# Optimization experiments

Measured on AMD Instinct MI355X. Metric: run time of the kernel, lower is better.

Reference implementation:

```python
import jax, jax.numpy as jnp
import numpy as np
from jax import lax

B, IN_C, OUT_C, Z_DIM, H, W = 16, 128, 128, 128, 64, 64
K, NUM_GROUPS, EPS = 3, 8, 1e-5


def setup_inputs() -> dict:
    key = jax.random.key(0)
    ks = jax.random.split(key, 10)
    s = 1.0 / np.sqrt(Z_DIM)
    return {
        "x": jax.random.normal(ks[0], (B, IN_C, H, W), dtype=jnp.float32),
        "z": jax.random.normal(ks[1], (B, Z_DIM), dtype=jnp.float32),
        # hypernet head for conv1: z_dim -> out_c*in_c*k*k
        "h1_w": jax.random.normal(ks[2], (Z_DIM, OUT_C * IN_C * K * K), dtype=jnp.float32) * s,
        "h1_b": jax.random.normal(ks[3], (OUT_C * IN_C * K * K,), dtype=jnp.float32) * 0.01,
        # hypernet head for conv2: z_dim -> out_c*out_c*k*k
        "h2_w": jax.random.normal(ks[4], (Z_DIM, OUT_C * OUT_C * K * K), dtype=jnp.float32) * s,
        "h2_b": jax.random.normal(ks[5], (OUT_C * OUT_C * K * K,), dtype=jnp.float32) * 0.01,
        "gamma1": jnp.ones((OUT_C,), dtype=jnp.float32),
        "beta1": jnp.zeros((OUT_C,), dtype=jnp.float32),
        "gamma2": jnp.ones((OUT_C,), dtype=jnp.float32),
        "beta2": jnp.zeros((OUT_C,), dtype=jnp.float32),
    }


def _per_sample_conv(x, w, stride, pad):
    # x: [B,C,H,W], w: [B,O,I,k,k] -> [B,O,H',W'] (per-sample weights)
    def one(xi, wi):
        return lax.conv_general_dilated(
            xi[None], wi, (stride, stride), [(pad, pad), (pad, pad)],
            dimension_numbers=("NCHW", "OIHW", "NCHW"))[0]
    return jax.vmap(one)(x, w)


def _group_norm(x, gamma, beta):
    b, c, h, w = x.shape
    xg = x.reshape(b, NUM_GROUPS, -1)
    mean = xg.mean(axis=-1, keepdims=True)
    var = xg.var(axis=-1, keepdims=True)
    xg = (xg - mean) * lax.rsqrt(var + EPS)
    x = xg.reshape(b, c, h, w)
    return x * gamma[None, :, None, None] + beta[None, :, None, None]


def reference(x, z, h1_w, h1_b, h2_w, h2_b, gamma1, beta1, gamma2, beta2):
    w1 = (z @ h1_w + h1_b).reshape(B, OUT_C, IN_C, K, K)
    out = _per_sample_conv(x, w1, 1, K // 2)
    out = jax.nn.relu(_group_norm(out, gamma1, beta1))
    w2 = (z @ h2_w + h2_b).reshape(B, OUT_C, OUT_C, K, K)
    out = _per_sample_conv(out, w2, 1, K // 2)
    out = _group_norm(out, gamma2, beta2)
    return jax.nn.relu(out + x)  # identity shortcut (stride=1, in_c==out_c)
```

## Files before the change

kernel.cpp:

```cpp
#include <hip/hip_runtime.h>

#define BB 16
#define CC 128
#define HH 64
#define WW 64
#define NG 8
#define WPB 147456
#define PLANE 4096
#define GROUP_N 65536.f

typedef __attribute__((ext_vector_type(8))) short short8;
typedef __attribute__((ext_vector_type(4))) float floatx4;
typedef __attribute__((ext_vector_type(4))) unsigned short ushortx4;

__device__ __forceinline__ unsigned short f2bf(float f) {
    unsigned u = __builtin_bit_cast(unsigned, f);
    return (unsigned short)((u + 0x7fffu + ((u >> 16) & 1u)) >> 16);
}
__device__ __forceinline__ float bf2f(unsigned short h) {
    unsigned u = ((unsigned)h) << 16;
    return __builtin_bit_cast(float, u);
}

__global__ __launch_bounds__(256)
void transpose_in(const float* __restrict__ x, unsigned short* __restrict__ xt)
{
    int blk = blockIdx.x;
    int b = blk >> 8, icc = (blk >> 6) & 3, y = blk & 63;
    int xi = threadIdx.x & 63, vg = threadIdx.x >> 6;
    const float* src = x + (((size_t)(b * CC + icc * 32 + vg * 8)) * HH + y) * WW + xi;
    short8 o;
#pragma unroll
    for (int e = 0; e < 8; ++e) o[e] = (short)f2bf(src[(size_t)e * PLANE]);
    unsigned short* dst = xt + (((size_t)(b * 4 + icc) * PLANE) + y * WW + xi) * 32 + vg * 8;
    *(short8*)dst = o;
}

__global__ __launch_bounds__(256)
void hyper_gemm(const float* __restrict__ z, const float* __restrict__ hw,
                const float* __restrict__ hb, unsigned short* __restrict__ wf)
{
    __shared__ float zs[BB * 128];
    __shared__ unsigned short wlds[BB][576];
    const int tid = threadIdx.x;
    for (int i = tid; i < BB * 128; i += 256) zs[i] = z[i];
    __syncthreads();

    const int oc = blockIdx.x >> 1, half = blockIdx.x & 1;
    const int base_n = oc * 1152 + half * 576;

    for (int c = 0; c < 3; ++c) {
        int nl = c * 256 + tid;
        if (nl < 576) {
            int n = base_n + nl;
            float acc[BB];
#pragma unroll
            for (int b = 0; b < BB; ++b) acc[b] = 0.f;
#pragma unroll 4
            for (int k = 0; k < 128; ++k) {
                float hv = hw[(size_t)k * WPB + n];
#pragma unroll
                for (int b = 0; b < BB; ++b) acc[b] += zs[b * 128 + k] * hv;
            }
            float bias = hb[n];
#pragma unroll
            for (int b = 0; b < BB; ++b) wlds[b][nl] = f2bf(acc[b] + bias);
        }
    }
    __syncthreads();

    const int frag = oc >> 4, lane_lo = oc & 15;
    for (int i = tid; i < 1152; i += 256) {
        int b = i / 72, r = i % 72;
        int icl = r / 36, r2 = r % 36;
        int tap = r2 >> 2, hi = r2 & 3;
        int icc = half * 2 + icl;
        short8 o;
#pragma unroll
        for (int j = 0; j < 8; ++j)
            o[j] = (short)wlds[b][(icl * 32 + hi * 8 + j) * 9 + tap];
        size_t off = ((((size_t)(b * 4 + icc) * 9 + tap) * 8 + frag) * 64 + (lane_lo | (hi << 4))) * 8;
        *(short8*)(wf + off) = o;
    }
}

template <int MODE>
__global__ __launch_bounds__(256, 2)
void conv_mfma(const unsigned short* __restrict__ xt,
               const unsigned short* __restrict__ wf,
               unsigned short* __restrict__ yt, float* __restrict__ ynchw,
               float* __restrict__ stats)
{
    const int blk = blockIdx.x;
    const int b = blk >> 5, tile = blk & 31;
    const int tid = threadIdx.x;
    const int w = tid >> 6, lane = tid & 63;
    const int i = w >> 1, j = w & 1;
    const int q = lane >> 4, n16 = lane & 15;
    const int y = tile * 2 + j;

    floatx4 acc[4][4];
#pragma unroll
    for (int mf = 0; mf < 4; ++mf)
#pragma unroll
        for (int nf = 0; nf < 4; ++nf) acc[mf][nf] = (floatx4)0.f;

    const unsigned short* xtb_b = xt + (size_t)b * 4 * PLANE * 32;
    const unsigned short* wf_b  = wf + (size_t)b * WPB;

    for (int icc = 0; icc < 4; ++icc) {
        const unsigned short* xtb = xtb_b + (size_t)icc * PLANE * 32;
        const unsigned short* wfc = wf_b + (size_t)icc * 36864;
#pragma unroll
        for (int tap = 0; tap < 9; ++tap) {
            const int dy = tap / 3 - 1, dx = tap % 3 - 1;
            const int yy = y + dy;
            if ((unsigned)yy >= (unsigned)HH) continue;

            short8 a[4], bbf[4];
#pragma unroll
            for (int mf = 0; mf < 4; ++mf)
                a[mf] = *(const short8*)(wfc + (((size_t)(tap * 8 + i * 4 + mf)) * 64 + lane) * 8);
#pragma unroll
            for (int nf = 0; nf < 4; ++nf) {
                int xx = nf * 16 + n16 + dx;
                if ((unsigned)xx < (unsigned)WW)
                    bbf[nf] = *(const short8*)(xtb + ((size_t)(yy * WW + xx)) * 32 + q * 8);
                else
                    bbf[nf] = (short8)0;
            }
#pragma unroll
            for (int mf = 0; mf < 4; ++mf)
#pragma unroll
                for (int nf = 0; nf < 4; ++nf)
                    acc[mf][nf] = __builtin_amdgcn_mfma_f32_16x16x32_bf16(
                        a[mf], bbf[nf], acc[mf][nf], 0, 0, 0);
        }
    }

#pragma unroll
    for (int mf = 0; mf < 4; ++mf) {
        float s1 = 0.f, s2 = 0.f;
#pragma unroll
        for (int nf = 0; nf < 4; ++nf) {
#pragma unroll
            for (int r = 0; r < 4; ++r) {
                float v = acc[mf][nf][r];
                s1 += v; s2 += v * v;
            }
            const int xx = nf * 16 + n16;
            if (MODE == 0) {
                const int icc1 = i * 2 + (mf >> 1);
                const int v0 = (mf & 1) * 16 + q * 4;
                unsigned short* p = yt + (((size_t)(b * 4 + icc1) * PLANE) + y * WW + xx) * 32 + v0;
                ushortx4 u;
                u.x = f2bf(acc[mf][nf][0]); u.y = f2bf(acc[mf][nf][1]);
                u.z = f2bf(acc[mf][nf][2]); u.w = f2bf(acc[mf][nf][3]);
                *(ushortx4*)p = u;
            } else {
#pragma unroll
                for (int r = 0; r < 4; ++r) {
                    int oc = i * 64 + mf * 16 + q * 4 + r;
                    ynchw[(((size_t)(b * CC + oc)) * HH + y) * WW + xx] = acc[mf][nf][r];
                }
            }
        }
#pragma unroll
        for (int off = 32; off > 0; off >>= 1) {
            s1 += __shfl_down(s1, off, 64);
            s2 += __shfl_down(s2, off, 64);
        }
        if (lane == 0) {
            int g = i * 4 + mf;
            atomicAdd(&stats[(b * NG + g) * 2 + 0], s1);
            atomicAdd(&stats[(b * NG + g) * 2 + 1], s2);
        }
    }
}

__global__ __launch_bounds__(256)
void norm_relu_bf16(unsigned short* __restrict__ yt, const float* __restrict__ stats,
                    const float* __restrict__ gamma, const float* __restrict__ beta)
{
    int idx8 = blockIdx.x * 256 + threadIdx.x;
    int t = idx8 >> 2;
    int bicc = t >> 12;
    int b = bicc >> 2, icc = bicc & 3;
    int cb = icc * 32 + (idx8 & 3) * 8;
    int g = cb >> 4;
    float sum = stats[(b * NG + g) * 2 + 0];
    float ssq = stats[(b * NG + g) * 2 + 1];
    float mean = sum * (1.f / GROUP_N);
    float var  = ssq * (1.f / GROUP_N) - mean * mean;
    float inv  = rsqrtf(var + 1e-5f);

    short8 d = *(short8*)(yt + (size_t)idx8 * 8);
    short8 o;
#pragma unroll
    for (int e = 0; e < 8; ++e) {
        float s = gamma[cb + e] * inv;
        float tt = beta[cb + e] - mean * s;
        float v = bf2f((unsigned short)d[e]);
        o[e] = (short)f2bf(fmaxf(v * s + tt, 0.f));
    }
    *(short8*)(yt + (size_t)idx8 * 8) = o;
}

__global__ __launch_bounds__(256)
void gn_add_relu(float* __restrict__ y2, const float* __restrict__ x,
                 const float* __restrict__ stats, const float* __restrict__ gamma,
                 const float* __restrict__ beta)
{
    const int bc = blockIdx.x;
    const int b = bc >> 7, c = bc & 127;
    const int g = c >> 4;
    float sum  = stats[(b * NG + g) * 2 + 0];
    float ssq  = stats[(b * NG + g) * 2 + 1];
    float mean = sum * (1.f / GROUP_N);
    float var  = ssq * (1.f / GROUP_N) - mean * mean;
    float inv  = rsqrtf(var + 1e-5f);
    float s = gamma[c] * inv;
    float t = beta[c] - mean * s;

    size_t base = (size_t)bc * PLANE;
    float4* yp = (float4*)(y2 + base);
    const float4* xp = (const float4*)(x + base);
    for (int i = threadIdx.x; i < PLANE / 4; i += 256) {
        float4 v = yp[i], xv = xp[i];
        v.x = fmaxf(v.x * s + t + xv.x, 0.f);
        v.y = fmaxf(v.y * s + t + xv.y, 0.f);
        v.z = fmaxf(v.z * s + t + xv.z, 0.f);
        v.w = fmaxf(v.w * s + t + xv.w, 0.f);
        yp[i] = v;
    }
}

extern "C" void kernel_launch(void* const* d_in, const int* in_sizes, int n_in,
                              void* d_out, int out_size, void* d_ws, size_t ws_size,
                              hipStream_t stream)
{
    const float* x   = (const float*)d_in[0];
    const float* z   = (const float*)d_in[1];
    const float* h1w = (const float*)d_in[2];
    const float* h1b = (const float*)d_in[3];
    const float* h2w = (const float*)d_in[4];
    const float* h2b = (const float*)d_in[5];
    const float* g1  = (const float*)d_in[6];
    const float* b1  = (const float*)d_in[7];
    const float* g2  = (const float*)d_in[8];
    const float* b2  = (const float*)d_in[9];
    float* out = (float*)d_out;

    float* stats1 = (float*)d_ws;
    float* stats2 = stats1 + 256;
    unsigned short* wfb = (unsigned short*)((char*)d_ws + 2048);
    unsigned short* xt0 = (unsigned short*)((char*)d_ws + 2048 + 4718592);
    unsigned short* xt1 = xt0 + 8388608;

    hipMemsetAsync(d_ws, 0, 2048, stream);

    transpose_in<<<4096, 256, 0, stream>>>(x, xt0);

    hyper_gemm<<<256, 256, 0, stream>>>(z, h1w, h1b, wfb);
    conv_mfma<0><<<512, 256, 0, stream>>>(xt0, wfb, xt1, nullptr, stats1);

    norm_relu_bf16<<<4096, 256, 0, stream>>>(xt1, stats1, g1, b1);

    hyper_gemm<<<256, 256, 0, stream>>>(z, h2w, h2b, wfb);
    conv_mfma<1><<<512, 256, 0, stream>>>(xt1, wfb, nullptr, out, stats2);

    gn_add_relu<<<2048, 256, 0, stream>>>(out, x, stats2, g2, b2);
}
```

Before: 458.3 us.

## Merge both hypernet GEMMs into one streaming launch plus separate repack kernel

```diff
diff --git a/kernel.cpp b/kernel.cpp
--- a/kernel.cpp
+++ b/kernel.cpp
@@ -37,49 +37,61 @@
 }
 
 __global__ __launch_bounds__(256)
-void hyper_gemm(const float* __restrict__ z, const float* __restrict__ hw,
-                const float* __restrict__ hb, unsigned short* __restrict__ wf)
-{
-    __shared__ float zs[BB * 128];
-    __shared__ unsigned short wlds[BB][576];
-    const int tid = threadIdx.x;
-    for (int i = tid; i < BB * 128; i += 256) zs[i] = z[i];
-    __syncthreads();
-
-    const int oc = blockIdx.x >> 1, half = blockIdx.x & 1;
-    const int base_n = oc * 1152 + half * 576;
-
-    for (int c = 0; c < 3; ++c) {
-        int nl = c * 256 + tid;
-        if (nl < 576) {
-            int n = base_n + nl;
-            float acc[BB];
-#pragma unroll
-            for (int b = 0; b < BB; ++b) acc[b] = 0.f;
-#pragma unroll 4
-            for (int k = 0; k < 128; ++k) {
-                float hv = hw[(size_t)k * WPB + n];
-#pragma unroll
-                for (int b = 0; b < BB; ++b) acc[b] += zs[b * 128 + k] * hv;
-            }
-            float bias = hb[n];
-#pragma unroll
-            for (int b = 0; b < BB; ++b) wlds[b][nl] = f2bf(acc[b] + bias);
-        }
-    }
-    __syncthreads();
-
-    const int frag = oc >> 4, lane_lo = oc & 15;
-    for (int i = tid; i < 1152; i += 256) {
-        int b = i / 72, r = i % 72;
-        int icl = r / 36, r2 = r % 36;
-        int tap = r2 >> 2, hi = r2 & 3;
-        int icc = half * 2 + icl;
+void stream_gemm(const float* __restrict__ z,
+                 const float* __restrict__ h1w, const float* __restrict__ h1b,
+                 const float* __restrict__ h2w, const float* __restrict__ h2b,
+                 unsigned short* __restrict__ P)
+{
+    const int blk = blockIdx.x;
+    const int which = (blk >= 576) ? 1 : 0;
+    const int n = (blk - which * 576) * 256 + threadIdx.x;
+    const float* __restrict__ hw = which ? h2w : h1w;
+    const float* __restrict__ hb = which ? h2b : h1b;
+    unsigned short* pw = P + (size_t)which * 2359296;
+
+    float acc[BB];
+#pragma unroll
+    for (int b = 0; b < BB; ++b) acc[b] = 0.f;
+
+    for (int k0 = 0; k0 < 128; k0 += 8) {
+        float hv[8];
+#pragma unroll
+        for (int u = 0; u < 8; ++u) hv[u] = hw[(size_t)(k0 + u) * WPB + n];
+#pragma unroll
+        for (int u = 0; u < 8; ++u) {
+#pragma unroll
+            for (int b = 0; b < BB; ++b)
+                acc[b] = fmaf(z[b * 128 + k0 + u], hv[u], acc[b]);
+        }
+    }
+    const float bias = hb[n];
+#pragma unroll
+    for (int b = 0; b < BB; ++b)
+        pw[(size_t)b * WPB + n] = f2bf(acc[b] + bias);
+}
+
+__global__ __launch_bounds__(256)
+void repack(const unsigned short* __restrict__ P,
+            unsigned short* __restrict__ wf1, unsigned short* __restrict__ wf2)
+{
+    int gid = blockIdx.x * 256 + threadIdx.x;
+    int which = gid >> 15, g = gid & 32767;
+    int lane = g & 63, frag = (g >> 6) & 7, icc = (g >> 9) & 3, b = g >> 11;
+
+    const unsigned short* src = P + (size_t)which * 2359296 + (size_t)b * WPB
+        + (frag * 16 + (lane & 15)) * 1152 + (icc * 32 + (lane >> 4) * 8) * 9;
+    unsigned short buf[72];
+#pragma unroll
+    for (int i = 0; i < 9; ++i)
+        *(short8*)(buf + i * 8) = *(const short8*)(src + i * 8);
+
+    unsigned short* wf = which ? wf2 : wf1;
+#pragma unroll
+    for (int tap = 0; tap < 9; ++tap) {
         short8 o;
 #pragma unroll
-        for (int j = 0; j < 8; ++j)
-            o[j] = (short)wlds[b][(icl * 32 + hi * 8 + j) * 9 + tap];
-        size_t off = ((((size_t)(b * 4 + icc) * 9 + tap) * 8 + frag) * 64 + (lane_lo | (hi << 4))) * 8;
+        for (int j = 0; j < 8; ++j) o[j] = (short)buf[j * 9 + tap];
+        size_t off = ((((size_t)(b * 4 + icc) * 9 + tap) * 8 + frag) * 64 + lane) * 8;
         *(short8*)(wf + off) = o;
     }
 }
@@ -253,21 +265,24 @@
 
     float* stats1 = (float*)d_ws;
     float* stats2 = stats1 + 256;
-    unsigned short* wfb = (unsigned short*)((char*)d_ws + 2048);
-    unsigned short* xt0 = (unsigned short*)((char*)d_ws + 2048 + 4718592);
+    unsigned short* wf1 = (unsigned short*)((char*)d_ws + 2048);
+    unsigned short* wf2 = wf1 + 2359296;
+    unsigned short* xt0 = wf2 + 2359296;
     unsigned short* xt1 = xt0 + 8388608;
+    unsigned short* P   = xt1;
 
     hipMemsetAsync(d_ws, 0, 2048, stream);
 
     transpose_in<<<4096, 256, 0, stream>>>(x, xt0);
 
-    hyper_gemm<<<256, 256, 0, stream>>>(z, h1w, h1b, wfb);
-    conv_mfma<0><<<512, 256, 0, stream>>>(xt0, wfb, xt1, nullptr, stats1);
+    stream_gemm<<<1152, 256, 0, stream>>>(z, h1w, h1b, h2w, h2b, P);
+    repack<<<256, 256, 0, stream>>>(P, wf1, wf2);
+
+    conv_mfma<0><<<512, 256, 0, stream>>>(xt0, wf1, xt1, nullptr, stats1);
 
     norm_relu_bf16<<<4096, 256, 0, stream>>>(xt1, stats1, g1, b1);
 
-    hyper_gemm<<<256, 256, 0, stream>>>(z, h2w, h2b, wfb);
-    conv_mfma<1><<<512, 256, 0, stream>>>(xt1, wfb, nullptr, out, stats2);
+    conv_mfma<1><<<512, 256, 0, stream>>>(xt1, wf2, nullptr, out, stats2);
 
     gn_add_relu<<<2048, 256, 0, stream>>>(out, x, stats2, g2, b2);
 }
```

Result: faster. 373.9 us (-18.4%).
